# Kernel optimization log

Hardware: AMD Instinct MI355X
Metric: run time of the kernel (lower is better)

## Reference

```python
import jax, jax.numpy as jnp
import numpy as np

B, N, D, H = 128, 256, 256, 4  # batch, atoms, feature dim (= fingerprint = input = output), heads
NEG_BIG = -1e10


def setup_inputs() -> dict:
    key = jax.random.key(0)
    ks = jax.random.split(key, 8)
    atom_neighbor_SNN = jax.random.normal(ks[0], (B, N, D), dtype=jnp.float32)
    # 0/1 adjacency (float): mask trick exp(x*-1e10)*-1e10 expects binary entries
    x_full_atom_neighbors = jax.random.randint(ks[1], (B, N, N), 0, 2).astype(jnp.float32)
    # shared neighbor_fc: Linear(D, D)
    lim = 1.0 / np.sqrt(D)
    fc_w = jax.random.uniform(ks[2], (D, D), jnp.float32, -lim, lim)
    fc_b = jnp.zeros((D,), jnp.float32)
    # per-head kernels (xavier_uniform)
    xav = np.sqrt(6.0 / (D + D))
    kernels = jax.random.uniform(ks[3], (H, D, D), jnp.float32, -xav, xav)
    # attention kernels (2D, 1) split into self/neigh halves, xavier on (2D,1)
    xav_a = np.sqrt(6.0 / (2 * D + 1))
    att_self = jax.random.uniform(ks[4], (H, D), jnp.float32, -xav_a, xav_a)
    att_neigh = jax.random.uniform(ks[5], (H, D), jnp.float32, -xav_a, xav_a)
    epsilons = jnp.full((H,), 0.6, jnp.float32)
    biases = jnp.zeros((H, D), jnp.float32)
    att_biases = jnp.zeros((H,), jnp.float32)
    return {
        "atom_neighbor_SNN": atom_neighbor_SNN,
        "x_full_atom_neighbors": x_full_atom_neighbors,
        "fc_w": fc_w, "fc_b": fc_b,
        "kernels": kernels,
        "att_self": att_self, "att_neigh": att_neigh,
        "epsilons": epsilons, "biases": biases, "att_biases": att_biases,
    }


def reference(atom_neighbor_SNN, x_full_atom_neighbors, fc_w, fc_b, kernels,
              att_self, att_neigh, epsilons, biases, att_biases):
    x = x_full_atom_neighbors                      # [B,N,N]
    atom = atom_neighbor_SNN                       # [B,N,D]
    diag = jnp.diagonal(x, axis1=-2, axis2=-1)     # [B,N]
    # new_x[h] = x + eye*diag*(eps[h]-1); so new_x[h] @ atom = x@atom + (eps[h]-1)*diag[:,:,None]*atom
    base = jnp.einsum('bnm,bmd->bnd', x, atom)     # [B,N,D]
    diagterm = diag[..., None] * atom              # [B,N,D]
    nf = base[None] + (epsilons - 1.0)[:, None, None, None] * diagterm[None]  # [H,B,N,D]
    h = jax.nn.leaky_relu(jnp.einsum('hbnd,df->hbnf', nf, fc_w) + fc_b, 0.01)  # shared fc, leaky_relu
    feat = jnp.einsum('hbnf,hfo->hbno', h, kernels) + biases[:, None, None, :]  # [H,B,N,D]
    a_s = jnp.einsum('hbno,ho->hbn', feat, att_self) + att_biases[:, None, None]
    a_n = jnp.einsum('hbno,ho->hbn', feat, att_neigh)
    att = jax.nn.elu(a_s[..., :, None] + a_n[..., None, :])  # [H,B,N,N]
    mask = jnp.exp(x * NEG_BIG) * NEG_BIG                     # 0 on edges, -1e10 off edges
    att = jax.nn.softmax(att + mask[None], axis=-1)
    # dropout: identity (eval mode)
    node = jnp.einsum('hbij,hbjo->hbio', att, feat)           # [H,B,N,D]
    out = jnp.moveaxis(node, 0, 2).reshape(node.shape[1], node.shape[2], H * node.shape[3])  # concat heads -> [B,N,H*D]
    return out, att[-1]
```

## Files before the change

### kernel.cpp

```cpp
#include <hip/hip_runtime.h>

typedef __attribute__((ext_vector_type(8))) short bf16x8;
typedef __attribute__((ext_vector_type(4))) short short4v;
typedef __attribute__((ext_vector_type(4))) float f32x4;


__device__ __forceinline__ float b2f(short s){
  unsigned u = ((unsigned)(unsigned short)s) << 16;
  return __builtin_bit_cast(float, u);
}
__device__ __forceinline__ short f2b(float f){
  unsigned u = __builtin_bit_cast(unsigned, f);
  u = (u + 0x7FFFu + ((u >> 16) & 1u)) >> 16;
  return (short)(unsigned short)u;
}

#define SWZ(row, bytecol) ((((row) * 512) + (bytecol)) ^ (((row) & 7) << 4))

__global__ __launch_bounds__(256) void ktrans(const float* __restrict__ fcw, const float* __restrict__ kers,
                                              short* __restrict__ WT, short* __restrict__ KhT){
  __shared__ float tile[32][33];
  int z = blockIdx.z;
  const float* src = (z == 0) ? fcw : (kers + (z-1)*65536);
  short* dst = (z == 0) ? WT : (KhT + (z-1)*65536);
  int x0 = blockIdx.x*32, y0 = blockIdx.y*32;
  int tx = threadIdx.x & 31, ty = threadIdx.x >> 5;
  #pragma unroll
  for (int i = 0; i < 32; i += 8) tile[ty+i][tx] = src[(y0+ty+i)*256 + x0+tx];
  __syncthreads();
  #pragma unroll
  for (int i = 0; i < 32; i += 8) dst[(x0+ty+i)*256 + y0+tx] = f2b(tile[tx][ty+i]);
}

__global__ __launch_bounds__(256) void kprep(const float* __restrict__ atom, const float* __restrict__ x,
                                             short* __restrict__ atom_bf, short* __restrict__ xbf,
                                             unsigned* __restrict__ xbits, float* __restrict__ diag){
  int b = blockIdx.y;
  int row = blockIdx.x*32 + (threadIdx.x >> 3);
  int seg = threadIdx.x & 7;
  if (blockIdx.z == 0){
    const float* p = atom + b*65536 + row*256 + seg*32;
    short* q = atom_bf + b*65536 + row*256 + seg*32;
    #pragma unroll
    for (int k = 0; k < 4; k++){
      f32x4 a = ((const f32x4*)p)[k*2], c = ((const f32x4*)p)[k*2+1];
      bf16x8 o;
      #pragma unroll
      for (int e = 0; e < 4; e++){ o[e] = f2b(a[e]); o[4+e] = f2b(c[e]); }
      ((bf16x8*)q)[k] = o;
    }
  } else {
    const float* p = x + b*65536 + row*256 + seg*32;
    float v[32];
    #pragma unroll
    for (int k = 0; k < 8; k++){
      f32x4 qv = ((const f32x4*)p)[k];
      #pragma unroll
      for (int e = 0; e < 4; e++) v[k*4+e] = qv[e];
    }
    unsigned bits = 0u;
    #pragma unroll
    for (int e = 0; e < 32; e++) if (v[e] > 0.5f) bits |= (1u << e);
    xbits[(b*256 + row)*8 + seg] = bits;
    short* q = xbf + b*65536 + row*256 + seg*32;
    #pragma unroll
    for (int k = 0; k < 4; k++){
      bf16x8 o;
      #pragma unroll
      for (int e = 0; e < 8; e++) o[e] = f2b(v[k*8+e]);
      ((bf16x8*)q)[k] = o;
    }
    if ((row >> 5) == seg) diag[b*256 + row] = v[row & 31];
  }
}

__global__ __launch_bounds__(512, 1) void kG12(const short* __restrict__ WT, const short* __restrict__ atomb,
                                               const short* __restrict__ xbf,
                                               short* __restrict__ G2nf, short* __restrict__ G1){
  __shared__ __align__(16) char G2s[65536];
  int wg = blockIdx.x;
  int xcd = wg & 7, idx = wg >> 3;
  int b  = xcd + ((idx >> 1) << 3);
  int fh = idx & 1;
  int tid = threadIdx.x, lane = tid & 63, w = tid >> 6;
  int lr = lane & 15, lq = lane >> 4, koff = lq * 8;

  {
    int wm = (w >> 1) * 64, wf = (w & 1) * 64;
    const short* Ab = atomb + b*65536;
    const short* Bw = WT + (fh*128 + wf)*256;
    f32x4 acc[4][4] = {};
    for (int k0 = 0; k0 < 256; k0 += 32){
      bf16x8 af[4], bfr[4];
      #pragma unroll
      for (int i = 0; i < 4; i++) af[i]  = *(const bf16x8*)(Ab + (wm + i*16 + lr)*256 + k0 + koff);
      #pragma unroll
      for (int j = 0; j < 4; j++) bfr[j] = *(const bf16x8*)(Bw + (j*16 + lr)*256 + k0 + koff);
      #pragma unroll
      for (int i = 0; i < 4; i++)
        #pragma unroll
        for (int j = 0; j < 4; j++)
          acc[i][j] = __builtin_amdgcn_mfma_f32_16x16x32_bf16(af[i], bfr[j], acc[i][j], 0, 0, 0);
    }
    #pragma unroll
    for (int i = 0; i < 4; i++)
      #pragma unroll
      for (int j = 0; j < 4; j++){
        short4v v;
        #pragma unroll
        for (int r = 0; r < 4; r++) v[r] = f2b(acc[i][j][r]);
        int fl = wf + j*16 + lr;
        int m0 = wm + i*16 + lq*4;
        *(short4v*)(G2s + SWZ(fl, m0*2)) = v;
        #pragma unroll
        for (int r = 0; r < 4; r++)
          G2nf[b*65536 + (m0 + r)*256 + fh*128 + fl] = v[r];
      }
  }
  __syncthreads();

  {
    int wf2 = (w >> 2) * 64, wn2 = (w & 3) * 64;
    const short* Xb = xbf + b*65536;
    f32x4 acc[4][4] = {};
    for (int k0 = 0; k0 < 256; k0 += 32){
      bf16x8 af[4], bfr[4];
      #pragma unroll
      for (int i = 0; i < 4; i++) af[i]  = *(const bf16x8*)(G2s + SWZ(wf2 + i*16 + lr, (k0 + koff)*2));
      #pragma unroll
      for (int j = 0; j < 4; j++) bfr[j] = *(const bf16x8*)(Xb + (wn2 + j*16 + lr)*256 + k0 + koff);
      #pragma unroll
      for (int i = 0; i < 4; i++)
        #pragma unroll
        for (int j = 0; j < 4; j++)
          acc[i][j] = __builtin_amdgcn_mfma_f32_16x16x32_bf16(af[i], bfr[j], acc[i][j], 0, 0, 0);
    }
    #pragma unroll
    for (int i = 0; i < 4; i++)
      #pragma unroll
      for (int j = 0; j < 4; j++){
        short4v v;
        #pragma unroll
        for (int r = 0; r < 4; r++) v[r] = f2b(acc[i][j][r]);
        *(short4v*)(G1 + b*65536 + (wn2 + j*16 + lr)*256 + fh*128 + wf2 + i*16 + lq*4) = v;
      }
  }
}

__global__ __launch_bounds__(512, 1) void kHead(const short* __restrict__ KhT, const short* __restrict__ G1,
                                                const short* __restrict__ G2nf, const float* __restrict__ diag,
                                                const float* __restrict__ fcb, const float* __restrict__ epsv,
                                                const float* __restrict__ biases, const float* __restrict__ atts,
                                                const float* __restrict__ attn, const float* __restrict__ attbv,
                                                const unsigned* __restrict__ xbits,
                                                float* __restrict__ out, float* __restrict__ out2){
  __shared__ __align__(16) char featS[131072];
  __shared__ __align__(16) char scratch[24576];
  __shared__ float asvL[256], anvL[256], fcbL[256];

  char* Pb0 = scratch;
  char* Pb1 = scratch + 8192;
  float (*red_s)[64] = (float(*)[64])(scratch + 16384);
  float (*red_n)[64] = (float(*)[64])(scratch + 16384 + 2048);
  unsigned* xbitsL = (unsigned*)(scratch + 16384);

  int wg = blockIdx.x;
  int xcd = wg & 7, idx = wg >> 3;
  int b = xcd + ((idx >> 2) << 3);
  int h = idx & 3;
  int tid = threadIdx.x, lane = tid & 63, w = tid >> 6;
  float epsm1 = epsv[h] - 1.0f;
  const short* KA  = KhT + h*65536;
  const short* G1b = G1  + b*65536;
  const short* G2b = G2nf + b*65536;

  {
    int o = tid >> 1, half = (tid & 1) * 128;
    #pragma unroll
    for (int q = 0; q < 16; q++){
      int kk = half + q*8;
      bf16x8 v = *(const bf16x8*)(KA + o*256 + kk);
      *(bf16x8*)(featS + SWZ(o, kk*2)) = v;
    }
    if (tid < 256) fcbL[tid] = fcb[tid];
  }

  int wro = (w >> 2) * 128;
  int wn  = (w & 3) * 64;
  int lr = lane & 15, lq = lane >> 4;
  int koff = lq * 8;
  float cj[4];
  #pragma unroll
  for (int j = 0; j < 4; j++) cj[j] = epsm1 * diag[b*256 + wn + j*16 + lr];

  __syncthreads();

  f32x4 acc[4][8] = {};
  for (int t = 0; t < 8; t++){
    int k0 = t*32;
    f32x4 fb0 = *(const f32x4*)&fcbL[k0 + koff];
    f32x4 fb1 = *(const f32x4*)&fcbL[k0 + koff + 4];
    bf16x8 af[4];
    #pragma unroll
    for (int j = 0; j < 4; j++){
      int row = wn + j*16 + lr;
      bf16x8 g1 = *(const bf16x8*)(G1b + row*256 + k0 + koff);
      bf16x8 g2 = *(const bf16x8*)(G2b + row*256 + k0 + koff);
      bf16x8 o;
      #pragma unroll
      for (int e = 0; e < 8; e++){
        float fbv = (e < 4) ? fb0[e] : fb1[e-4];
        float v = b2f(g1[e]) + cj[j]*b2f(g2[e]) + fbv;
        v = v > 0.f ? v : 0.01f*v;
        o[e] = f2b(v);
      }
      af[j] = o;
    }
    #pragma unroll
    for (int i = 0; i < 8; i++){
      bf16x8 bfv = *(const bf16x8*)(featS + SWZ(wro + i*16 + lr, (k0 + koff)*2));
      #pragma unroll
      for (int j = 0; j < 4; j++)
        acc[j][i] = __builtin_amdgcn_mfma_f32_16x16x32_bf16(af[j], bfv, acc[j][i], 0, 0, 0);
    }
  }
  __syncthreads();

  float ps[4][4] = {}, pn[4][4] = {};
  #pragma unroll
  for (int i = 0; i < 8; i++){
    int od = wro + i*16 + lr;
    float bi  = biases[h*256 + od];
    float wsv = atts[h*256 + od];
    float wnv = attn[h*256 + od];
    #pragma unroll
    for (int j = 0; j < 4; j++){
      short4v sv;
      #pragma unroll
      for (int r = 0; r < 4; r++){
        float fv = acc[j][i][r] + bi;
        sv[r] = f2b(fv);
        ps[j][r] += fv * wsv;
        pn[j][r] += fv * wnv;
      }
      *(short4v*)(featS + SWZ(od, (wn + j*16 + lq*4)*2) ) = sv;
    }
  }
  #pragma unroll
  for (int j = 0; j < 4; j++)
    #pragma unroll
    for (int r = 0; r < 4; r++){
      float s = ps[j][r], nv = pn[j][r];
      s += __shfl_xor(s, 1); s += __shfl_xor(s, 2); s += __shfl_xor(s, 4); s += __shfl_xor(s, 8);
      nv += __shfl_xor(nv, 1); nv += __shfl_xor(nv, 2); nv += __shfl_xor(nv, 4); nv += __shfl_xor(nv, 8);
      ps[j][r] = s; pn[j][r] = nv;
    }
  if (lr == 0){
    #pragma unroll
    for (int j = 0; j < 4; j++)
      #pragma unroll
      for (int r = 0; r < 4; r++){
        red_s[w][j*16 + lq*4 + r] = ps[j][r];
        red_n[w][j*16 + lq*4 + r] = pn[j][r];
      }
  }
  __syncthreads();
  if (tid < 256){
    int q = tid >> 6, nn = tid & 63;
    asvL[tid] = red_s[q][nn] + red_s[q+4][nn] + attbv[h];
    anvL[tid] = red_n[q][nn] + red_n[q+4][nn];
  }
  __syncthreads();
  {
    const unsigned* xb = xbits + b*2048;
    #pragma unroll
    for (int q = 0; q < 4; q++) xbitsL[tid*4 + q] = xb[tid*4 + q];
  }
  __syncthreads();

  int row = tid >> 5, seg = tid & 31;
  {
    int i = row;
    float as_i = asvL[i];
    unsigned bits = xbitsL[i*8 + (seg >> 2)];
    int sh = (seg & 3) * 8;
    float Lv[8]; float mx = -3.0e38f;
    #pragma unroll
    for (int e = 0; e < 8; e++){
      float s = as_i + anvL[seg*8 + e];
      float el = s > 0.f ? s : (__expf(s) - 1.0f);
      float L = el + (((bits >> (sh + e)) & 1u) ? 0.f : -1.0e10f);
      Lv[e] = L; mx = fmaxf(mx, L);
    }
    mx = fmaxf(mx, __shfl_xor(mx, 1)); mx = fmaxf(mx, __shfl_xor(mx, 2));
    mx = fmaxf(mx, __shfl_xor(mx, 4)); mx = fmaxf(mx, __shfl_xor(mx, 8));
    mx = fmaxf(mx, __shfl_xor(mx, 16));
    float sum = 0.f;
    #pragma unroll
    for (int e = 0; e < 8; e++){ float p = __expf(Lv[e] - mx); Lv[e] = p; sum += p; }
    sum += __shfl_xor(sum, 1); sum += __shfl_xor(sum, 2); sum += __shfl_xor(sum, 4);
    sum += __shfl_xor(sum, 8); sum += __shfl_xor(sum, 16);
    float inv = 1.0f / sum;
    bf16x8 pv;
    #pragma unroll
    for (int e = 0; e < 8; e++) pv[e] = f2b(Lv[e] * inv);
    *(bf16x8*)(Pb0 + SWZ(row, seg*16)) = pv;
    if (h == 3){
      float* o2 = out2 + b*65536 + i*256 + seg*8;
      f32x4 v0, v1;
      #pragma unroll
      for (int e = 0; e < 4; e++){ v0[e] = Lv[e]*inv; v1[e] = Lv[4+e]*inv; }
      *(f32x4*)(o2) = v0; *(f32x4*)(o2 + 4) = v1;
    }
  }

  int o0w = w * 32;
  for (int t = 0; t < 16; t++){
    __syncthreads();
    int it0 = t * 16;
    char* Pr = (t & 1) ? Pb1 : Pb0;
    f32x4 a2[2] = {};
    for (int k0 = 0; k0 < 256; k0 += 32){
      bf16x8 bfp = *(const bf16x8*)(Pr + SWZ(lr, (k0 + koff)*2));
      #pragma unroll
      for (int ii = 0; ii < 2; ii++){
        bf16x8 afv = *(const bf16x8*)(featS + SWZ(o0w + ii*16 + lr, (k0 + koff)*2));
        a2[ii] = __builtin_amdgcn_mfma_f32_16x16x32_bf16(afv, bfp, a2[ii], 0, 0, 0);
      }
    }
    #pragma unroll
    for (int ii = 0; ii < 2; ii++)
      *(f32x4*)(out + (size_t)(b*256 + it0 + lr)*1024 + h*256 + o0w + ii*16 + lq*4) = a2[ii];

    if (t < 15){
      char* Pw = (t & 1) ? Pb0 : Pb1;
      int i = it0 + 16 + row;
      float as_i = asvL[i];
      unsigned bits = xbitsL[i*8 + (seg >> 2)];
      int sh = (seg & 3) * 8;
      float Lv[8]; float mx = -3.0e38f;
      #pragma unroll
      for (int e = 0; e < 8; e++){
        float s = as_i + anvL[seg*8 + e];
        float el = s > 0.f ? s : (__expf(s) - 1.0f);
        float L = el + (((bits >> (sh + e)) & 1u) ? 0.f : -1.0e10f);
        Lv[e] = L; mx = fmaxf(mx, L);
      }
      mx = fmaxf(mx, __shfl_xor(mx, 1)); mx = fmaxf(mx, __shfl_xor(mx, 2));
      mx = fmaxf(mx, __shfl_xor(mx, 4)); mx = fmaxf(mx, __shfl_xor(mx, 8));
      mx = fmaxf(mx, __shfl_xor(mx, 16));
      float sum = 0.f;
      #pragma unroll
      for (int e = 0; e < 8; e++){ float p = __expf(Lv[e] - mx); Lv[e] = p; sum += p; }
      sum += __shfl_xor(sum, 1); sum += __shfl_xor(sum, 2); sum += __shfl_xor(sum, 4);
      sum += __shfl_xor(sum, 8); sum += __shfl_xor(sum, 16);
      float inv = 1.0f / sum;
      bf16x8 pv;
      #pragma unroll
      for (int e = 0; e < 8; e++) pv[e] = f2b(Lv[e] * inv);
      *(bf16x8*)(Pw + SWZ(row, seg*16)) = pv;
      if (h == 3){
        float* o2 = out2 + b*65536 + i*256 + seg*8;
        f32x4 v0, v1;
        #pragma unroll
        for (int e = 0; e < 4; e++){ v0[e] = Lv[e]*inv; v1[e] = Lv[4+e]*inv; }
        *(f32x4*)(o2) = v0; *(f32x4*)(o2 + 4) = v1;
      }
    }
  }
}

extern "C" void kernel_launch(void* const* d_in, const int* in_sizes, int n_in,
                              void* d_out, int out_size, void* d_ws, size_t ws_size,
                              hipStream_t stream) {
  const float* atom   = (const float*)d_in[0];
  const float* x      = (const float*)d_in[1];
  const float* fc_w   = (const float*)d_in[2];
  const float* fc_b   = (const float*)d_in[3];
  const float* kers   = (const float*)d_in[4];
  const float* att_s  = (const float*)d_in[5];
  const float* att_n  = (const float*)d_in[6];
  const float* eps    = (const float*)d_in[7];
  const float* biases = (const float*)d_in[8];
  const float* att_b  = (const float*)d_in[9];

  char* w = (char*)d_ws;
  short* WT      = (short*)(w);
  short* KhT     = (short*)(w + 131072);
  float* diag    = (float*)(w + 655360);
  unsigned* xbits= (unsigned*)(w + 786432);
  short* atomb   = (short*)(w + 1835008);
  short* xbf     = (short*)(w + 18612224);
  short* G2nf    = (short*)(w + 35389440);
  short* G1      = (short*)(w + 52166656);

  float* out  = (float*)d_out;
  float* out2 = out + 33554432;

  ktrans<<<dim3(8, 8, 5), 256, 0, stream>>>(fc_w, kers, WT, KhT);
  kprep<<<dim3(8, 128, 2), 256, 0, stream>>>(atom, x, atomb, xbf, xbits, diag);
  kG12<<<dim3(256), 512, 0, stream>>>(WT, atomb, xbf, G2nf, G1);
  kHead<<<dim3(512), 512, 0, stream>>>(KhT, G1, G2nf, diag, fc_b, eps,
                                       biases, att_s, att_n, att_b, xbits, out, out2);
}
```

Measured before the change: 171.2 us.

## Stage leaky-ReLU activation tile in LDS once per K-step and prefetch next slice

The kHead GEMM prologue used to have every wave recompute the fc+bias+leaky_relu activation for its rows straight from global memory. Because the two wave groups share the same rows, that work and those loads were done twice. Now each thread computes a 16-element piece of a 256x32 activation tile once per K-step, writes it to an LDS buffer, and reads the MFMA A-fragments back from LDS. The next K-slice of G1/G2 is prefetched into registers while the MFMAs run. The cost is two extra block-wide barriers per K-iteration plus one extra barrier before reusing the scratch area for reductions.

Result: faster. 164.8 us (-3.7%).

```diff
diff --git a/kernel.cpp b/kernel.cpp
--- a/kernel.cpp
+++ b/kernel.cpp
@@ -158,6 +158,7 @@
   __shared__ __align__(16) char scratch[24576];
   __shared__ float asvL[256], anvL[256], fcbL[256];
 
+  short (*h1s)[40] = (short(*)[40])scratch;
   char* Pb0 = scratch;
   char* Pb1 = scratch + 8192;
   float (*red_s)[64] = (float(*)[64])(scratch + 16384);
@@ -185,37 +186,52 @@
     if (tid < 256) fcbL[tid] = fcb[tid];
   }
 
+  int nl = tid >> 1, rkk = (tid & 1) * 16;
+  float cj = epsm1 * diag[b*256 + nl];
+
   int wro = (w >> 2) * 128;
   int wn  = (w & 3) * 64;
   int lr = lane & 15, lq = lane >> 4;
   int koff = lq * 8;
-  float cj[4];
-  #pragma unroll
-  for (int j = 0; j < 4; j++) cj[j] = epsm1 * diag[b*256 + wn + j*16 + lr];
+
+  bf16x8 p1a = *(const bf16x8*)(G1b + nl*256 + rkk);
+  bf16x8 p1b = *(const bf16x8*)(G1b + nl*256 + rkk + 8);
+  bf16x8 p2a = *(const bf16x8*)(G2b + nl*256 + rkk);
+  bf16x8 p2b = *(const bf16x8*)(G2b + nl*256 + rkk + 8);
 
   __syncthreads();
 
   f32x4 acc[4][8] = {};
   for (int t = 0; t < 8; t++){
     int k0 = t*32;
-    f32x4 fb0 = *(const f32x4*)&fcbL[k0 + koff];
-    f32x4 fb1 = *(const f32x4*)&fcbL[k0 + koff + 4];
+    {
+      bf16x8 o1, o2;
+      #pragma unroll
+      for (int e = 0; e < 8; e++){
+        float v = b2f(p1a[e]) + cj*b2f(p2a[e]) + fcbL[k0 + rkk + e];
+        v = v > 0.f ? v : 0.01f*v;
+        o1[e] = f2b(v);
+      }
+      #pragma unroll
+      for (int e = 0; e < 8; e++){
+        float v = b2f(p1b[e]) + cj*b2f(p2b[e]) + fcbL[k0 + rkk + 8 + e];
+        v = v > 0.f ? v : 0.01f*v;
+        o2[e] = f2b(v);
+      }
+      *(bf16x8*)&h1s[nl][rkk] = o1;
+      *(bf16x8*)&h1s[nl][rkk + 8] = o2;
+    }
+    __syncthreads();
+    if (t < 7){
+      int kn = k0 + 32;
+      p1a = *(const bf16x8*)(G1b + nl*256 + kn + rkk);
+      p1b = *(const bf16x8*)(G1b + nl*256 + kn + rkk + 8);
+      p2a = *(const bf16x8*)(G2b + nl*256 + kn + rkk);
+      p2b = *(const bf16x8*)(G2b + nl*256 + kn + rkk + 8);
+    }
     bf16x8 af[4];
     #pragma unroll
-    for (int j = 0; j < 4; j++){
-      int row = wn + j*16 + lr;
-      bf16x8 g1 = *(const bf16x8*)(G1b + row*256 + k0 + koff);
-      bf16x8 g2 = *(const bf16x8*)(G2b + row*256 + k0 + koff);
-      bf16x8 o;
-      #pragma unroll
-      for (int e = 0; e < 8; e++){
-        float fbv = (e < 4) ? fb0[e] : fb1[e-4];
-        float v = b2f(g1[e]) + cj[j]*b2f(g2[e]) + fbv;
-        v = v > 0.f ? v : 0.01f*v;
-        o[e] = f2b(v);
-      }
-      af[j] = o;
-    }
+    for (int j = 0; j < 4; j++) af[j] = *(const bf16x8*)&h1s[wn + j*16 + lr][koff];
     #pragma unroll
     for (int i = 0; i < 8; i++){
       bf16x8 bfv = *(const bf16x8*)(featS + SWZ(wro + i*16 + lr, (k0 + koff)*2));
@@ -223,8 +239,8 @@
       for (int j = 0; j < 4; j++)
         acc[j][i] = __builtin_amdgcn_mfma_f32_16x16x32_bf16(af[j], bfv, acc[j][i], 0, 0, 0);
     }
-  }
-  __syncthreads();
+    __syncthreads();
+  }
 
   float ps[4][4] = {}, pn[4][4] = {};
   #pragma unroll
@@ -255,6 +271,7 @@
       nv += __shfl_xor(nv, 1); nv += __shfl_xor(nv, 2); nv += __shfl_xor(nv, 4); nv += __shfl_xor(nv, 8);
       ps[j][r] = s; pn[j][r] = nv;
     }
+  __syncthreads();
   if (lr == 0){
     #pragma unroll
     for (int j = 0; j < 4; j++)
```
